# Performance work log

Hardware: AMD Instinct MI355X
Metric: run time of the kernel (lower is better)

## Reference

```python
import jax, jax.numpy as jnp
import numpy as np

ANCHORS = jnp.array([[116.0, 90.0], [156.0, 198.0], [373.0, 326.0]], dtype=jnp.float32)
NUM_CLASSES = 80
IMG_SIZE = 416
EXP_CLAMP = 1000.0


def setup_inputs() -> dict:
    key = jax.random.key(0)
    # (batch, num_anchor*(num_classes+5), G, G) = (64, 255, 52, 52)
    X = jax.random.normal(key, (64, 255, 52, 52), dtype=jnp.float32)
    return {"X": X}


def reference(X):
    B = X.shape[0]
    G = X.shape[2]
    A = ANCHORS.shape[0]
    C = NUM_CLASSES
    ratio = IMG_SIZE / G  # stride

    # (B, A, 5+C, G, G) -> (B, A, G, G, 5+C)
    pred = X.reshape(B, A, C + 5, G, G).transpose(0, 1, 3, 4, 2)

    x = jax.nn.sigmoid(pred[..., 0])
    y = jax.nn.sigmoid(pred[..., 1])
    w = pred[..., 2]
    h = pred[..., 3]
    conf = jax.nn.sigmoid(pred[..., 4])
    clss = pred[..., 5:]  # raw logits, matching the torch module

    grid = jnp.arange(G, dtype=jnp.float32)
    coor_x = grid.reshape(1, 1, 1, G)   # varies along last (column) axis
    coor_y = grid.reshape(1, 1, G, 1)   # varies along row axis

    scale_anchors = ANCHORS / ratio
    anchor_x = scale_anchors[:, 0].reshape(1, A, 1, 1)
    anchor_y = scale_anchors[:, 1].reshape(1, A, 1, 1)

    bx = x + coor_x
    by = y + coor_y
    bw = jnp.minimum(jnp.exp(w), EXP_CLAMP) * anchor_x
    bh = jnp.minimum(jnp.exp(h), EXP_CLAMP) * anchor_y
    pred_boxes = jnp.stack([bx, by, bw, bh], axis=-1)  # (B, A, G, G, 4)

    output = jnp.concatenate(
        [
            pred_boxes.reshape(B, -1, 4) * ratio,
            conf.reshape(B, -1, 1),
            clss.reshape(B, -1, C),
        ],
        axis=-1,
    )  # (B, A*G*G, 5+C)
    return output
```

## Files before the change

kernel.cpp:

```cpp
#include <hip/hip_runtime.h>
#include <math.h>


constexpr int G    = 52;
constexpr int GG   = G * G;
constexpr int NA   = 3;
constexpr int NC   = 85;
constexpr int TILE = G;
constexpr int NT   = GG / TILE;
constexpr int NV   = TILE / 4;
constexpr int ITEMS = NC * NV;
constexpr int WORDS = TILE * NC;
constexpr int VOUT  = WORDS / 4;
constexpr float RATIO = 8.0f;

typedef float f32x4 __attribute__((ext_vector_type(4)));

__device__ __forceinline__ float sigmoidf_(float v) {
    return 1.0f / (1.0f + expf(-v));
}

__device__ __forceinline__ float transform_(float v, int c, float fj, float fi,
                                            float ax, float ay) {
    if (c >= 5) return v;
    if (c == 0) return (sigmoidf_(v) + fj) * RATIO;
    if (c == 1) return (sigmoidf_(v) + fi) * RATIO;
    if (c == 2) return fminf(expf(v), 1000.0f) * ax;
    if (c == 3) return fminf(expf(v), 1000.0f) * ay;
    return sigmoidf_(v);
}

__global__ __launch_bounds__(256)
void yolo_head_kernel(const float* __restrict__ X, float* __restrict__ out) {
    __shared__ float lds[WORDS];

    const int bid  = blockIdx.x;
    const int tile = bid % NT;
    const int ba   = bid / NT;
    const int a    = ba % NA;
    const int b    = ba / NA;

    const float fi = (float)tile;
    const float ax = (a == 0) ? 116.0f : ((a == 1) ? 156.0f : 373.0f);
    const float ay = (a == 0) ?  90.0f : ((a == 1) ? 198.0f : 326.0f);

    const f32x4* src = reinterpret_cast<const f32x4*>(
        X + ((size_t)(b * NA + a) * NC) * GG + (size_t)tile * TILE);
    const int srow = GG / 4;

    const int tid = threadIdx.x;

    #pragma unroll
    for (int it = 0; it < 5; ++it) {
        const int idx = tid + it * 256;
        if (it < 4 || idx < ITEMS) {
            const int c  = idx / NV;
            const int v4 = idx - c * NV;
            f32x4 val = src[(size_t)c * srow + v4];
            const int j0 = v4 << 2;
            #pragma unroll
            for (int m = 0; m < 4; ++m) {
                lds[(j0 + m) * NC + c] =
                    transform_(val[m], c, (float)(j0 + m), fi, ax, ay);
            }
        }
    }

    __syncthreads();

    f32x4* dst4 = reinterpret_cast<f32x4*>(
        out + ((size_t)(b * NA + a) * GG + (size_t)tile * TILE) * NC);
    const f32x4* lds4 = reinterpret_cast<const f32x4*>(lds);

    #pragma unroll
    for (int it = 0; it < 5; ++it) {
        const int idx = tid + it * 256;
        if (it < 4 || idx < VOUT) {
            __builtin_nontemporal_store(lds4[idx], &dst4[idx]);
        }
    }
}

extern "C" void kernel_launch(void* const* d_in, const int* in_sizes, int n_in,
                              void* d_out, int out_size, void* d_ws, size_t ws_size,
                              hipStream_t stream) {
    const float* X = (const float*)d_in[0];
    float* out = (float*)d_out;
    const int B = in_sizes[0] / (NA * NC * GG);
    dim3 grid((unsigned)(B * NA * NT));
    yolo_head_kernel<<<grid, dim3(256), 0, stream>>>(X, out);
}
```

Measured before the change: 71.43 us.

## Split transpose into per-wavefront 16-row tiles without block barrier

Each wavefront now independently transposes a 16-position by 85-channel tile through its own LDS slice, and the block-wide __syncthreads is replaced by a compiler memory barrier. Box transforms run only in the first iteration, for the lanes holding channels 0-4, and all other channels are copied raw. The aim is to remove block synchronisation and branchy per-element transform work, and to give finer-grained parallelism with smaller LDS per wave. It relies on wavefront-synchronous execution for LDS visibility, and global reads become 64-byte segments per channel row, which may be less efficient.

```diff
diff --git a/kernel.cpp b/kernel.cpp
--- a/kernel.cpp
+++ b/kernel.cpp
@@ -2,16 +2,12 @@
 #include <math.h>
 
 
-constexpr int G    = 52;
-constexpr int GG   = G * G;
-constexpr int NA   = 3;
-constexpr int NC   = 85;
-constexpr int TILE = G;
-constexpr int NT   = GG / TILE;
-constexpr int NV   = TILE / 4;
-constexpr int ITEMS = NC * NV;
-constexpr int WORDS = TILE * NC;
-constexpr int VOUT  = WORDS / 4;
+constexpr int G   = 52;
+constexpr int GG  = G * G;
+constexpr int NA  = 3;
+constexpr int NC  = 85;
+constexpr int RPW = 16;
+constexpr int WTB = GG / RPW;
 constexpr float RATIO = 8.0f;
 
 typedef float f32x4 __attribute__((ext_vector_type(4)));
@@ -20,62 +16,67 @@
     return 1.0f / (1.0f + expf(-v));
 }
 
-__device__ __forceinline__ float transform_(float v, int c, float fj, float fi,
-                                            float ax, float ay) {
-    if (c >= 5) return v;
-    if (c == 0) return (sigmoidf_(v) + fj) * RATIO;
-    if (c == 1) return (sigmoidf_(v) + fi) * RATIO;
-    if (c == 2) return fminf(expf(v), 1000.0f) * ax;
-    if (c == 3) return fminf(expf(v), 1000.0f) * ay;
-    return sigmoidf_(v);
-}
+__global__ __launch_bounds__(256)
+void yolo_head_kernel(const float* __restrict__ X, float* __restrict__ out,
+                      int total_wt) {
+    __shared__ float lds[4 * RPW * NC];
 
-__global__ __launch_bounds__(256)
-void yolo_head_kernel(const float* __restrict__ X, float* __restrict__ out) {
-    __shared__ float lds[WORDS];
+    const int w    = threadIdx.x >> 6;
+    const int lane = threadIdx.x & 63;
+    const int t    = blockIdx.x * 4 + w;
+    if (t >= total_wt) return;
 
-    const int bid  = blockIdx.x;
-    const int tile = bid % NT;
-    const int ba   = bid / NT;
-    const int a    = ba % NA;
-    const int b    = ba / NA;
+    const int ba  = t / WTB;
+    const int rem = t - ba * WTB;
+    const int ij0 = rem * RPW;
 
-    const float fi = (float)tile;
+    const int a = ba % NA;
     const float ax = (a == 0) ? 116.0f : ((a == 1) ? 156.0f : 373.0f);
     const float ay = (a == 0) ?  90.0f : ((a == 1) ? 198.0f : 326.0f);
 
-    const f32x4* src = reinterpret_cast<const f32x4*>(
-        X + ((size_t)(b * NA + a) * NC) * GG + (size_t)tile * TILE);
-    const int srow = GG / 4;
+    const f32x4* src = reinterpret_cast<const f32x4*>(X)
+                       + (size_t)ba * NC * (GG / 4) + (ij0 >> 2);
+    float* ldsw = lds + w * (RPW * NC);
 
-    const int tid = threadIdx.x;
+    const int c0 = lane >> 2;
+    const int v4 = lane & 3;
+    const int jl = v4 << 2;
 
     #pragma unroll
-    for (int it = 0; it < 5; ++it) {
-        const int idx = tid + it * 256;
-        if (it < 4 || idx < ITEMS) {
-            const int c  = idx / NV;
-            const int v4 = idx - c * NV;
-            f32x4 val = src[(size_t)c * srow + v4];
-            const int j0 = v4 << 2;
-            #pragma unroll
-            for (int m = 0; m < 4; ++m) {
-                lds[(j0 + m) * NC + c] =
-                    transform_(val[m], c, (float)(j0 + m), fi, ax, ay);
+    for (int it = 0; it < 6; ++it) {
+        if (it < 5 || lane < 20) {
+            const int c = it * 16 + c0;
+            f32x4 val = src[(size_t)c * (GG / 4) + v4];
+            if (it == 0 && lane < 20) {
+                #pragma unroll
+                for (int m = 0; m < 4; ++m) {
+                    const int ij = ij0 + jl + m;
+                    const float v = val[m];
+                    float r;
+                    if (c == 0)      r = (sigmoidf_(v) + (float)(ij % G)) * RATIO;
+                    else if (c == 1) r = (sigmoidf_(v) + (float)(ij / G)) * RATIO;
+                    else if (c == 2) r = fminf(expf(v), 1000.0f) * ax;
+                    else if (c == 3) r = fminf(expf(v), 1000.0f) * ay;
+                    else             r = sigmoidf_(v);
+                    ldsw[(jl + m) * NC + c] = r;
+                }
+            } else {
+                #pragma unroll
+                for (int m = 0; m < 4; ++m)
+                    ldsw[(jl + m) * NC + c] = val[m];
             }
         }
     }
 
-    __syncthreads();
+    asm volatile("" ::: "memory");
 
-    f32x4* dst4 = reinterpret_cast<f32x4*>(
-        out + ((size_t)(b * NA + a) * GG + (size_t)tile * TILE) * NC);
-    const f32x4* lds4 = reinterpret_cast<const f32x4*>(lds);
-
+    const f32x4* lds4 = reinterpret_cast<const f32x4*>(ldsw);
+    f32x4* dst4 = reinterpret_cast<f32x4*>(out)
+                  + (size_t)ba * (GG * NC / 4) + (size_t)rem * (RPW * NC / 4);
     #pragma unroll
-    for (int it = 0; it < 5; ++it) {
-        const int idx = tid + it * 256;
-        if (it < 4 || idx < VOUT) {
+    for (int it = 0; it < 6; ++it) {
+        const int idx = it * 64 + lane;
+        if (it < 5 || lane < 20) {
             __builtin_nontemporal_store(lds4[idx], &dst4[idx]);
         }
     }
@@ -87,6 +88,7 @@
     const float* X = (const float*)d_in[0];
     float* out = (float*)d_out;
     const int B = in_sizes[0] / (NA * NC * GG);
-    dim3 grid((unsigned)(B * NA * NT));
-    yolo_head_kernel<<<grid, dim3(256), 0, stream>>>(X, out);
+    const int total_wt = B * NA * WTB;
+    const int blocks = (total_wt + 3) / 4;
+    yolo_head_kernel<<<dim3((unsigned)blocks), dim3(256), 0, stream>>>(X, out, total_wt);
 }
```

New measurement: 64.75 us. 1.1x faster.
